# Optimization experiments

Measured on AMD Instinct MI355X. Metric: run time of the kernel, lower is better.

Reference implementation:

```python
import jax, jax.numpy as jnp
import numpy as np

B, H, W, C = 16, 56, 56, 384
NH, WS = 12, 7
N = WS * WS
NW = (H // WS) * (W // WS)
SHIFTS = (0, WS // 2)
HD = C // NH
SCALE = HD ** -0.5


def _rel_idx():
    ch, cw = np.meshgrid(np.arange(WS), np.arange(WS), indexing='ij')
    cf = np.stack([ch.ravel(), cw.ravel()])            # (2, N)
    rc = cf[:, :, None] - cf[:, None, :]               # (2, N, N)
    rc = rc.transpose(1, 2, 0).copy()
    rc[:, :, 0] += WS - 1
    rc[:, :, 1] += WS - 1
    rc[:, :, 0] *= 2 * WS - 1
    return rc.sum(-1).astype(np.int32)                 # (N, N)


def _attn_mask(shift):
    img = np.zeros((H, W))
    sl = (slice(0, -WS), slice(-WS, -shift), slice(-shift, None))
    cnt = 0
    for hs in sl:
        for ws_ in sl:
            img[hs, ws_] = cnt
            cnt += 1
    mw = img.reshape(H // WS, WS, W // WS, WS).transpose(0, 2, 1, 3).reshape(-1, N)
    d = mw[:, None, :] - mw[:, :, None]
    return np.where(d != 0, -100.0, 0.0).astype(np.float32)  # (NW, N, N)


def setup_inputs() -> dict:
    key = jax.random.key(0)
    ks = jax.random.split(key, 8)
    p = lambda k, shape: (jax.random.normal(k, shape, jnp.float32) * 0.02)
    return dict(
        x=jax.random.normal(ks[0], (B, H, W, C), jnp.float32),
        attn_mask=jnp.asarray(_attn_mask(SHIFTS[1])),
        rel_idx=jnp.asarray(_rel_idx()),
        norm1_g=jnp.ones((2, C), jnp.float32),
        norm1_b=jnp.zeros((2, C), jnp.float32),
        qkv_w=p(ks[1], (2, 3 * C, C)),
        qkv_b=jnp.zeros((2, 3 * C), jnp.float32),
        rpb=p(ks[2], (2, (2 * WS - 1) ** 2, NH)),
        proj_w=p(ks[3], (2, C, C)),
        proj_b=jnp.zeros((2, C), jnp.float32),
        norm2_g=jnp.ones((2, C), jnp.float32),
        norm2_b=jnp.zeros((2, C), jnp.float32),
        fc1_w=p(ks[4], (2, 4 * C, C)),
        fc1_b=jnp.zeros((2, 4 * C), jnp.float32),
        fc2_w=p(ks[5], (2, C, 4 * C)),
        fc2_b=jnp.zeros((2, C), jnp.float32),
    )


def _ln(x, g, b):
    m = x.mean(-1, keepdims=True)
    v = x.var(-1, keepdims=True)
    return (x - m) * jax.lax.rsqrt(v + 1e-5) * g + b


def _partition(x):
    # (B,H,W,C) -> (B*nW, N, C)
    x = x.reshape(B, H // WS, WS, W // WS, WS, C)
    return x.transpose(0, 1, 3, 2, 4, 5).reshape(-1, N, C)


def _reverse(w):
    # (B*nW, N, C) -> (B,H,W,C)
    w = w.reshape(B, H // WS, W // WS, WS, WS, C)
    return w.transpose(0, 1, 3, 2, 4, 5).reshape(B, H, W, C)


def reference(x, attn_mask, rel_idx, norm1_g, norm1_b, qkv_w, qkv_b, rpb,
              proj_w, proj_b, norm2_g, norm2_b, fc1_w, fc1_b, fc2_w, fc2_b):
    for i, shift in enumerate(SHIFTS):
        shortcut = x.reshape(B, H * W, C)
        xn = _ln(shortcut, norm1_g[i], norm1_b[i]).reshape(B, H, W, C)
        if shift > 0:
            xn = jnp.roll(xn, (-shift, -shift), (1, 2))
        xw = _partition(xn)                               # (B_, N, C)
        qkv = xw @ qkv_w[i].T + qkv_b[i]                  # (B_, N, 3C)
        qkv = qkv.reshape(-1, N, 3, NH, HD).transpose(2, 0, 3, 1, 4)
        q, k, v = qkv[0], qkv[1], qkv[2]                  # (B_, NH, N, HD)
        attn = jnp.einsum('bhnd,bhmd->bhnm', q * SCALE, k)
        bias = rpb[i][rel_idx.reshape(-1)].reshape(N, N, NH).transpose(2, 0, 1)
        attn = attn + bias[None]
        if shift > 0:
            attn = attn.reshape(B, NW, NH, N, N) + attn_mask[None, :, None]
            attn = attn.reshape(-1, NH, N, N)
        attn = jax.nn.softmax(attn, axis=-1)
        out = jnp.einsum('bhnm,bhmd->bhnd', attn, v)
        out = out.transpose(0, 2, 1, 3).reshape(-1, N, C)
        out = out @ proj_w[i].T + proj_b[i]
        sx = _reverse(out)
        if shift > 0:
            sx = jnp.roll(sx, (shift, shift), (1, 2))
        x = shortcut + sx.reshape(B, H * W, C)
        h = jax.nn.gelu(_ln(x, norm2_g[i], norm2_b[i]) @ fc1_w[i].T + fc1_b[i],
                        approximate=False)
        x = x + (h @ fc2_w[i].T + fc2_b[i])
        x = x.reshape(B, H, W, C)
    return x
```

## Files before the change

### kernel.cpp

```cpp
#include <hip/hip_runtime.h>
#include <hip/hip_fp8.h>
#include <math.h>

typedef unsigned char  u8;
typedef unsigned short u16;
typedef unsigned int   u32;
typedef long long      i64;
typedef __attribute__((ext_vector_type(4))) float f32x4;
typedef __attribute__((ext_vector_type(8))) short bf16x8;

#define M_TOK 50176
#define CDIM  384

__device__ __forceinline__ u16 f2b(float f){
  union { float f; u32 u; } v; v.f = f;
  u32 r = v.u + 0x7fffu + ((v.u >> 16) & 1u);
  return (u16)(r >> 16);
}
__device__ __forceinline__ u32 pack2(float a, float b){
  return (u32)f2b(a) | ((u32)f2b(b) << 16);
}
__device__ __forceinline__ u8 f2q(float v){
  __hip_fp8_e4m3 t(v);
  return *reinterpret_cast<u8*>(&t);
}

__device__ __forceinline__ void gload_lds16(const void* g, void* l){
  __builtin_amdgcn_global_load_lds((const __attribute__((address_space(1))) u32*)g,
                                   (__attribute__((address_space(3))) u32*)l, 16, 0, 0);
}

__global__ void cvtw(const float* __restrict__ in, u16* __restrict__ out, int n4){
  int i = blockIdx.x * 256 + threadIdx.x;
  if (i < n4){
    float4 v = ((const float4*)in)[i];
    uint2 o; o.x = pack2(v.x, v.y); o.y = pack2(v.z, v.w);
    ((uint2*)out)[i] = o;
  }
}
__global__ void cvtw8(const float* __restrict__ in, u8* __restrict__ out, int n4){
  int i = blockIdx.x * 256 + threadIdx.x;
  if (i < n4){
    float4 v = ((const float4*)in)[i];
    u32 o = (u32)f2q(v.x) | ((u32)f2q(v.y) << 8) |
            ((u32)f2q(v.z) << 16) | ((u32)f2q(v.w) << 24);
    ((u32*)out)[i] = o;
  }
}

template<int F8>
__global__ __launch_bounds__(256) void ln_kernel(
    const float* __restrict__ x, const float* __restrict__ g,
    const float* __restrict__ b, void* __restrict__ out, int ntok)
{
  int wave = threadIdx.x >> 6, lane = threadIdx.x & 63;
  for (long t = blockIdx.x * 4 + wave; t < ntok; t += (long)gridDim.x * 4){
    const float* xr = x + t * CDIM;
    float v[6]; float s = 0.f, ss = 0.f;
    #pragma unroll
    for (int j = 0; j < 6; ++j){ v[j] = xr[j*64 + lane]; s += v[j]; ss += v[j]*v[j]; }
    #pragma unroll
    for (int o = 32; o >= 1; o >>= 1){ s += __shfl_xor(s, o); ss += __shfl_xor(ss, o); }
    float mean = s * (1.f/384.f);
    float var  = ss * (1.f/384.f) - mean*mean;
    float rs   = rsqrtf(var + 1e-5f);
    #pragma unroll
    for (int j = 0; j < 6; ++j){
      int c = j*64 + lane;
      float val = (v[j] - mean) * rs * g[c] + b[c];
      if (F8) ((u8*)out)[t*CDIM + c] = f2q(val);
      else    ((u16*)out)[t*CDIM + c] = f2b(val);
    }
  }
}

template<int EPI>
__global__ __launch_bounds__(256, 4) void gemm_bt(
    const u16* __restrict__ A, const u16* __restrict__ Wt,
    const float* __restrict__ bias, const float* __restrict__ resid,
    void* __restrict__ outp, int M, int N, int K)
{
  __shared__ __align__(16) u16 smem[16384];
  const int tid  = threadIdx.x;
  const int wave = tid >> 6, lane = tid & 63;
  const int nbn  = N >> 7;
  const int nwg = gridDim.x;
  const int q8 = nwg >> 3, r8 = nwg & 7, xcd = blockIdx.x & 7, o8 = blockIdx.x >> 3;
  const int sid = (xcd < r8 ? xcd*(q8+1) : r8*(q8+1) + (xcd-r8)*q8) + o8;
  const int bm = sid / nbn, bn = sid % nbn;
  const int wr = wave >> 1, wc = wave & 1;
  const int l15 = lane & 15, l4 = lane >> 4;
  const int srow = tid >> 2, sch = tid & 3;

  f32x4 acc[4][4] = {};

  auto STAGE = [&](int buf, int kt){
    u16* lAp = smem + buf*4096;
    u16* lBp = smem + 8192 + buf*4096;
    #pragma unroll
    for (int it = 0; it < 2; ++it){
      int row = it*64 + srow;
      int chs = sch ^ ((srow >> 1) & 3);
      const u16* ga = A  + (size_t)(bm*128 + row) * K + kt + chs*8;
      const u16* gb = Wt + (size_t)(bn*128 + row) * K + kt + chs*8;
      gload_lds16(ga, &lAp[(it*256 + wave*64) * 8]);
      gload_lds16(gb, &lBp[(it*256 + wave*64) * 8]);
    }
  };

  const int NK = K >> 5;
  STAGE(0, 0);

  int cur = 0;
  for (int ki = 0; ki < NK; ++ki){
    if (ki + 1 < NK){
      STAGE(cur ^ 1, (ki + 1) * 32);
      asm volatile("s_waitcnt vmcnt(4)" ::: "memory");
    } else {
      asm volatile("s_waitcnt vmcnt(0)" ::: "memory");
    }
    __builtin_amdgcn_s_barrier();
    const u16* lAp = smem + cur*4096;
    const u16* lBp = smem + 8192 + cur*4096;
    bf16x8 af[4], bfr[4];
    const int rc = (l4 ^ ((l15 >> 1) & 3)) * 8;
    #pragma unroll
    for (int mi = 0; mi < 4; ++mi)
      af[mi] = *(const bf16x8*)&lAp[(wr*64 + mi*16 + l15)*32 + rc];
    #pragma unroll
    for (int ni = 0; ni < 4; ++ni)
      bfr[ni] = *(const bf16x8*)&lBp[(wc*64 + ni*16 + l15)*32 + rc];
    #pragma unroll
    for (int mi = 0; mi < 4; ++mi)
      #pragma unroll
      for (int ni = 0; ni < 4; ++ni)
        acc[mi][ni] = __builtin_amdgcn_mfma_f32_16x16x32_bf16(af[mi], bfr[ni], acc[mi][ni], 0, 0, 0);
    __builtin_amdgcn_s_barrier();
    cur ^= 1;
  }

  if (EPI == 2){
    #pragma unroll
    for (int ni = 0; ni < 4; ++ni){
      int col = bn*128 + wc*64 + ni*16 + l15;
      float bb = bias[col];
      #pragma unroll
      for (int mi = 0; mi < 4; ++mi){
        int row0 = bm*128 + wr*64 + mi*16 + l4*4;
        #pragma unroll
        for (int r = 0; r < 4; ++r){
          long off = (long)(row0 + r) * N + col;
          ((float*)outp)[off] = resid[off] + acc[mi][ni][r] + bb;
        }
      }
    }
  } else {
    #pragma unroll
    for (int ni = 0; ni < 4; ++ni){
      int colL = wc*64 + ni*16 + l15;
      float bb = bias[bn*128 + colL];
      int colS = colL ^ (l4*16);
      #pragma unroll
      for (int mi = 0; mi < 4; ++mi){
        int rowL = wr*64 + mi*16 + l4*4;
        #pragma unroll
        for (int r = 0; r < 4; ++r){
          float v = acc[mi][ni][r] + bb;
          smem[(rowL + r)*128 + colS] = f2b(v);
        }
      }
    }
    __syncthreads();
    const u32* eb = (const u32*)smem;
    u32* og = (u32*)outp;
    const int nW = N >> 1;
    #pragma unroll
    for (int it = 0; it < 32; ++it){
      int row = wave*32 + it;
      u32 w = eb[row*64 + (lane ^ (((row >> 2) & 3) * 8))];
      __builtin_nontemporal_store(w, &og[(size_t)(bm*128 + row) * nW + bn*64 + lane]);
    }
  }
}

template<int EPI>
__global__ __launch_bounds__(256, 4) void gemm_f8(
    const u8* __restrict__ A, const u8* __restrict__ Wt,
    const float* __restrict__ bias, const float* __restrict__ resid,
    void* __restrict__ outp, int M, int N, int K)
{
  __shared__ __align__(16) u8 smem[17408];
  const int tid  = threadIdx.x;
  const int wave = tid >> 6, lane = tid & 63;
  const int nbn  = N >> 7;
  const int nwg = gridDim.x;
  const int q8 = nwg >> 3, r8 = nwg & 7, xcd = blockIdx.x & 7, o8 = blockIdx.x >> 3;
  const int sid = (xcd < r8 ? xcd*(q8+1) : r8*(q8+1) + (xcd-r8)*q8) + o8;
  const int bm = sid / nbn, bn = sid % nbn;
  const int wr = wave >> 1, wc = wave & 1;
  const int l15 = lane & 15, l4 = lane >> 4;

  f32x4 acc[4][4] = {};

  const int gsl = tid ^ ((tid >> 3) & 7);
  const int grow = gsl >> 1, gc16 = gsl & 1;

  auto STAGE = [&](int buf, int kt){
    const u8* ga = A  + (size_t)(bm*128 + grow) * K + kt + gc16*16;
    const u8* gb = Wt + (size_t)(bn*128 + grow) * K + kt + gc16*16;
    gload_lds16(ga, &smem[buf*8192 + tid*16]);
    gload_lds16(gb, &smem[buf*8192 + 4096 + tid*16]);
  };

  const int NK = K >> 5;
  STAGE(0, 0);

  const int c16 = l4 >> 1, half8 = (l4 & 1) * 8;
  int spA[4], spB[4];
  #pragma unroll
  for (int mi = 0; mi < 4; ++mi){
    int s = (wr*64 + mi*16 + l15)*2 + c16;
    spA[mi] = (s ^ ((s >> 3) & 7)) * 16 + half8;
  }
  #pragma unroll
  for (int ni = 0; ni < 4; ++ni){
    int s = (wc*64 + ni*16 + l15)*2 + c16;
    spB[ni] = (s ^ ((s >> 3) & 7)) * 16 + half8;
  }

  int cur = 0;
  for (int ki = 0; ki < NK; ++ki){
    if (ki + 1 < NK){
      STAGE(cur ^ 1, (ki + 1) * 32);
      asm volatile("s_waitcnt vmcnt(2)" ::: "memory");
    } else {
      asm volatile("s_waitcnt vmcnt(0)" ::: "memory");
    }
    __builtin_amdgcn_s_barrier();
    const u8* lAp = smem + cur*8192;
    const u8* lBp = smem + cur*8192 + 4096;
    i64 af[4], bf[4];
    #pragma unroll
    for (int mi = 0; mi < 4; ++mi)
      af[mi] = *(const i64*)&lAp[spA[mi]];
    #pragma unroll
    for (int ni = 0; ni < 4; ++ni)
      bf[ni] = *(const i64*)&lBp[spB[ni]];
    #pragma unroll
    for (int mi = 0; mi < 4; ++mi)
      #pragma unroll
      for (int ni = 0; ni < 4; ++ni)
        acc[mi][ni] = __builtin_amdgcn_mfma_f32_16x16x32_fp8_fp8(af[mi], bf[ni], acc[mi][ni], 0, 0, 0);
    __builtin_amdgcn_s_barrier();
    cur ^= 1;
  }

  if (EPI == 2){
    #pragma unroll
    for (int ni = 0; ni < 4; ++ni){
      int col = bn*128 + wc*64 + ni*16 + l15;
      float bb = bias[col];
      #pragma unroll
      for (int mi = 0; mi < 4; ++mi){
        int row0 = bm*128 + wr*64 + mi*16 + l4*4;
        #pragma unroll
        for (int r = 0; r < 4; ++r){
          long off = (long)(row0 + r) * N + col;
          ((float*)outp)[off] = resid[off] + acc[mi][ni][r] + bb;
        }
      }
    }
  } else {
    #pragma unroll
    for (int ni = 0; ni < 4; ++ni){
      int col = wc*64 + ni*16 + l15;
      float bb = bias[bn*128 + col];
      #pragma unroll
      for (int mi = 0; mi < 4; ++mi){
        int row0 = wr*64 + mi*16 + l4*4;
        #pragma unroll
        for (int r = 0; r < 4; ++r){
          float v = acc[mi][ni][r] + bb;
          v = 0.5f * v * (1.f + erff(v * 0.70710678118654752f));
          smem[(row0 + r)*132 + col] = f2q(v);
        }
      }
    }
    __syncthreads();
    u32* og = (u32*)outp;
    const int nW = N >> 2;
    const int colu = tid & 31, rw = tid >> 5;
    #pragma unroll
    for (int it = 0; it < 16; ++it){
      int row = it*8 + rw;
      u32 w = *(const u32*)&smem[row*132 + colu*4];
      __builtin_nontemporal_store(w, &og[(size_t)(bm*128 + row) * nW + bn*32 + colu]);
    }
  }
}

__global__ void build_btbl(const float* __restrict__ rpb, const int* __restrict__ ridx,
                           float* __restrict__ btbl){
  int q = blockIdx.x & 63, h = blockIdx.x >> 6;
  int l = threadIdx.x;
  float v = -1e9f;
  if (q < 49){
    int key = (l & 3) * 16 + (l >> 2);
    if (key < 49) v = rpb[ridx[q*49 + key] * 12 + h];
  }
  btbl[(h*64 + q)*64 + l] = v;
}

template<int SHIFT>
__global__ __launch_bounds__(64) void attn_mfma(
    const u16* __restrict__ qkv, const float* __restrict__ btbl,
    u16* __restrict__ attn_out)
{
  __shared__ __align__(16) u16 p_lds[64*72];
  __shared__ __align__(16) u16 vt_lds[32*72];
  __shared__ int tok_lds[64];
  __shared__ int rid_lds[64];

  const int bid = blockIdx.x;
  const int h   = bid % 12;
  const int win = bid / 12;
  const int b   = win >> 6, wl = win & 63;
  const int wy  = wl >> 3,  wx = wl & 7;
  const int lane = threadIdx.x;
  const int l15 = lane & 15, l4 = lane >> 4;

  auto tokof = [&](int n)->int{
    int r = (n * 9363) >> 16;
    int c = n - r * 7;
    int hh = wy*7 + r + SHIFT; if (hh >= 56) hh -= 56;
    int ww = wx*7 + c + SHIFT; if (ww >= 56) ww -= 56;
    return b*3136 + hh*56 + ww;
  };

  {
    const int n  = lane;
    const int nc = n < 49 ? n : 48;
    const int t  = tokof(nc);
    tok_lds[n] = t;
    if (SHIFT){
      int r = (nc * 9363) >> 16, c = nc - r*7;
      int gh = wy*7 + r, gw = wx*7 + c;
      int rh = gh <= 48 ? 0 : (gh <= 52 ? 1 : 2);
      int rw = gw <= 48 ? 0 : (gw <= 52 ? 1 : 2);
      rid_lds[n] = rh*3 + rw;
    }
    const uint4* vp = (const uint4*)(qkv + (size_t)t*1152 + 768 + h*32);
    u32 w[16];
    #pragma unroll
    for (int j4 = 0; j4 < 4; ++j4){
      uint4 u = vp[j4];
      w[j4*4+0]=u.x; w[j4*4+1]=u.y; w[j4*4+2]=u.z; w[j4*4+3]=u.w;
    }
    if (n >= 49){
      #pragma unroll
      for (int j = 0; j < 16; ++j) w[j] = 0;
    }
    #pragma unroll
    for (int j = 0; j < 16; ++j){
      vt_lds[(2*j  )*72 + n] = (u16)(w[j] & 0xffffu);
      vt_lds[(2*j+1)*72 + n] = (u16)(w[j] >> 16);
    }
  }

  bf16x8 qa[4], kb[4];
  #pragma unroll
  for (int mi = 0; mi < 4; ++mi){
    int row = mi*16 + l15; int t = tokof(row < 49 ? row : 48);
    qa[mi] = *(const bf16x8*)(qkv + (size_t)t*1152 + h*32 + l4*8);
  }
  #pragma unroll
  for (int ni = 0; ni < 4; ++ni){
    int row = ni*16 + l15; int t = tokof(row < 49 ? row : 48);
    kb[ni] = *(const bf16x8*)(qkv + (size_t)t*1152 + 384 + h*32 + l4*8);
  }
  f32x4 s[4][4] = {};
  #pragma unroll
  for (int mi = 0; mi < 4; ++mi)
    #pragma unroll
    for (int ni = 0; ni < 4; ++ni)
      s[mi][ni] = __builtin_amdgcn_mfma_f32_16x16x32_bf16(qa[mi], kb[ni], s[mi][ni], 0, 0, 0);

  __syncthreads();

  int rid_k[4];
  if (SHIFT){
    #pragma unroll
    for (int ni = 0; ni < 4; ++ni) rid_k[ni] = rid_lds[ni*16 + l15];
  }

  const float* bt = btbl + h*4096;
  float den[4][4];
  #pragma unroll
  for (int mi = 0; mi < 4; ++mi){
    #pragma unroll
    for (int r = 0; r < 4; ++r){
      int q = mi*16 + l4*4 + r;
      f32x4 bq = *(const f32x4*)(bt + q*64 + l15*4);
      int ridq = 0;
      if (SHIFT) ridq = rid_lds[q];
      #pragma unroll
      for (int ni = 0; ni < 4; ++ni){
        float v = s[mi][ni][r] * 0.17677669529663687f + bq[ni];
        if (SHIFT) v += (ridq == rid_k[ni]) ? 0.f : -100.f;
        s[mi][ni][r] = v;
      }
      float m0 = fmaxf(fmaxf(s[mi][0][r], s[mi][1][r]), fmaxf(s[mi][2][r], s[mi][3][r]));
      #pragma unroll
      for (int o = 1; o <= 8; o <<= 1) m0 = fmaxf(m0, __shfl_xor(m0, o));
      float d0 = 0.f;
      #pragma unroll
      for (int ni = 0; ni < 4; ++ni){
        float e = __expf(s[mi][ni][r] - m0);
        s[mi][ni][r] = e; d0 += e;
      }
      #pragma unroll
      for (int o = 1; o <= 8; o <<= 1) d0 += __shfl_xor(d0, o);
      den[mi][r] = d0;
    }
  }

  #pragma unroll
  for (int mi = 0; mi < 4; ++mi)
    #pragma unroll
    for (int r = 0; r < 4; ++r){
      int q = mi*16 + l4*4 + r;
      #pragma unroll
      for (int ni = 0; ni < 4; ++ni)
        p_lds[q*72 + ni*16 + l15] = f2b(s[mi][ni][r]);
    }

  __syncthreads();

  f32x4 o2[4][2] = {};
  #pragma unroll
  for (int ks = 0; ks < 2; ++ks){
    bf16x8 vb[2];
    #pragma unroll
    for (int ni = 0; ni < 2; ++ni)
      vb[ni] = *(const bf16x8*)&vt_lds[(ni*16 + l15)*72 + ks*32 + l4*8];
    #pragma unroll
    for (int mi = 0; mi < 4; ++mi){
      bf16x8 pa = *(const bf16x8*)&p_lds[(mi*16 + l15)*72 + ks*32 + l4*8];
      #pragma unroll
      for (int ni = 0; ni < 2; ++ni)
        o2[mi][ni] = __builtin_amdgcn_mfma_f32_16x16x32_bf16(pa, vb[ni], o2[mi][ni], 0, 0, 0);
    }
  }

  #pragma unroll
  for (int mi = 0; mi < 4; ++mi){
    #pragma unroll
    for (int r = 0; r < 4; ++r){
      int q = mi*16 + l4*4 + r;
      if (q < 49){
        float inv = 1.f / den[mi][r];
        long t = tok_lds[q];
        #pragma unroll
        for (int ni = 0; ni < 2; ++ni){
          int d = ni*16 + l15;
          attn_out[t*384 + h*32 + d] = f2b(o2[mi][ni][r] * inv);
        }
      }
    }
  }
}

extern "C" void kernel_launch(void* const* d_in, const int* in_sizes, int n_in,
                              void* d_out, int out_size, void* d_ws, size_t ws_size,
                              hipStream_t stream)
{
  const float* x_in   = (const float*)d_in[0];
  const int*   relidx = (const int*)d_in[2];
  const float* n1g    = (const float*)d_in[3];
  const float* n1b    = (const float*)d_in[4];
  const float* qkvw   = (const float*)d_in[5];
  const float* qkvb   = (const float*)d_in[6];
  const float* rpb    = (const float*)d_in[7];
  const float* pw     = (const float*)d_in[8];
  const float* pb     = (const float*)d_in[9];
  const float* n2g    = (const float*)d_in[10];
  const float* n2b    = (const float*)d_in[11];
  const float* f1w    = (const float*)d_in[12];
  const float* f1b    = (const float*)d_in[13];
  const float* f2w    = (const float*)d_in[14];
  const float* f2bb   = (const float*)d_in[15];
  float* xout = (float*)d_out;

  char* ws = (char*)d_ws;
  u16* wqkv   = (u16*)ws; ws += (size_t)2*1152*384*2;
  u16* wproj  = (u16*)ws; ws += (size_t)2*384*384*2;
  u8*  wfc1q  = (u8*)ws;  ws += (size_t)2*1536*384;
  u8*  wfc2q  = (u8*)ws;  ws += (size_t)2*384*1536;
  u16* bufA   = (u16*)ws; ws += (size_t)M_TOK*1536*2;
  u16* bufB   = (u16*)ws; ws += (size_t)M_TOK*384*2;
  u8*  bufD   = (u8*)ws;  ws += (size_t)M_TOK*384;
  float* btbl = (float*)(bufA + (size_t)M_TOK*1152);
  u8* h8 = (u8*)bufA;

  {
    int n;
    n = 2*1152*384;  cvtw <<<dim3((n/4+255)/256), dim3(256), 0, stream>>>(qkvw, wqkv,  n/4);
    n = 2*384*384;   cvtw <<<dim3((n/4+255)/256), dim3(256), 0, stream>>>(pw,   wproj, n/4);
    n = 2*1536*384;  cvtw8<<<dim3((n/4+255)/256), dim3(256), 0, stream>>>(f1w,  wfc1q, n/4);
    n = 2*384*1536;  cvtw8<<<dim3((n/4+255)/256), dim3(256), 0, stream>>>(f2w,  wfc2q, n/4);
  }

  for (int i = 0; i < 2; ++i){
    const float* xi = (i == 0) ? x_in : xout;
    ln_kernel<0><<<dim3(2048), dim3(256), 0, stream>>>(xi, n1g + i*384, n1b + i*384, bufB, M_TOK);
    gemm_bt<0><<<dim3(3528), dim3(256), 0, stream>>>(
        bufB, wqkv + (size_t)i*1152*384, qkvb + i*1152, nullptr, bufA, M_TOK, 1152, 384);
    build_btbl<<<dim3(768), dim3(64), 0, stream>>>(rpb + (size_t)i*169*12, relidx, btbl);
    if (i == 0)
      attn_mfma<0><<<dim3(12288), dim3(64), 0, stream>>>(bufA, btbl, bufB);
    else
      attn_mfma<3><<<dim3(12288), dim3(64), 0, stream>>>(bufA, btbl, bufB);
    gemm_bt<2><<<dim3(1176), dim3(256), 0, stream>>>(
        bufB, wproj + (size_t)i*384*384, pb + i*384, xi, xout, M_TOK, 384, 384);
    ln_kernel<1><<<dim3(2048), dim3(256), 0, stream>>>(xout, n2g + i*384, n2b + i*384, bufD, M_TOK);
    gemm_f8<1><<<dim3(4704), dim3(256), 0, stream>>>(
        bufD, wfc1q + (size_t)i*1536*384, f1b + i*1536, nullptr, h8, M_TOK, 1536, 384);
    gemm_f8<2><<<dim3(1176), dim3(256), 0, stream>>>(
        h8, wfc2q + (size_t)i*384*1536, f2bb + i*384, xout, xout, M_TOK, 384, 1536);
  }
  (void)in_sizes; (void)n_in; (void)out_size; (void)ws_size;
}
```

Measured before the change: 929.1 us.

## Store fc1 GELU output directly with permuted fc2 weight layout, tanh GELU

The fc1 epilogue now packs four fp8 GELU outputs per lane straight into a 32-bit global store instead of staging through shared memory and a barrier. The packed columns are interleaved with stride 16, so the fc2 fp8 weights are re-laid out with a matching permutation along K to keep the contraction correct. The exact erf GELU is replaced by the tanh approximation using a fast exp, which cuts epilogue ALU work but slightly changes numerics. The global stores become 4-byte scattered per lane rather than row-coalesced, which may hurt write efficiency.

```diff
diff --git a/kernel.cpp b/kernel.cpp
--- a/kernel.cpp
+++ b/kernel.cpp
@@ -23,6 +23,12 @@
 __device__ __forceinline__ u8 f2q(float v){
   __hip_fp8_e4m3 t(v);
   return *reinterpret_cast<u8*>(&t);
+}
+__device__ __forceinline__ float gelu(float x){
+  float u = x * (0.7978845608028654f + 0.035677408136300125f * x * x);
+  float e = __expf(2.f * u);
+  float th = 1.f - 2.f / (e + 1.f);
+  return 0.5f * x * (1.f + th);
 }
 
 __device__ __forceinline__ void gload_lds16(const void* g, void* l){
@@ -45,6 +51,19 @@
     u32 o = (u32)f2q(v.x) | ((u32)f2q(v.y) << 8) |
             ((u32)f2q(v.z) << 16) | ((u32)f2q(v.w) << 24);
     ((u32*)out)[i] = o;
+  }
+}
+__global__ void cvtw8p(const float* __restrict__ in, u8* __restrict__ out,
+                       int rows, int cols){
+  int idx = blockIdx.x * 256 + threadIdx.x;
+  if (idx < rows * (cols >> 2)){
+    int byte0 = idx << 2;
+    int row = byte0 / cols, cb = byte0 % cols;
+    int g = cb >> 6, s = (cb & 63) >> 2;
+    const float* rp = in + (size_t)row * cols + g*64;
+    u32 w = (u32)f2q(rp[s]) | ((u32)f2q(rp[16 + s]) << 8) |
+            ((u32)f2q(rp[32 + s]) << 16) | ((u32)f2q(rp[48 + s]) << 24);
+    ((u32*)out)[idx] = w;
   }
 }
 
@@ -189,7 +208,7 @@
     const float* __restrict__ bias, const float* __restrict__ resid,
     void* __restrict__ outp, int M, int N, int K)
 {
-  __shared__ __align__(16) u8 smem[17408];
+  __shared__ __align__(16) u8 smem[16384];
   const int tid  = threadIdx.x;
   const int wave = tid >> 6, lane = tid & 63;
   const int nbn  = N >> 7;
@@ -271,30 +290,25 @@
       }
     }
   } else {
-    #pragma unroll
-    for (int ni = 0; ni < 4; ++ni){
-      int col = wc*64 + ni*16 + l15;
-      float bb = bias[bn*128 + col];
-      #pragma unroll
-      for (int mi = 0; mi < 4; ++mi){
-        int row0 = wr*64 + mi*16 + l4*4;
-        #pragma unroll
-        for (int r = 0; r < 4; ++r){
-          float v = acc[mi][ni][r] + bb;
-          v = 0.5f * v * (1.f + erff(v * 0.70710678118654752f));
-          smem[(row0 + r)*132 + col] = f2q(v);
-        }
-      }
-    }
-    __syncthreads();
     u32* og = (u32*)outp;
     const int nW = N >> 2;
-    const int colu = tid & 31, rw = tid >> 5;
-    #pragma unroll
-    for (int it = 0; it < 16; ++it){
-      int row = it*8 + rw;
-      u32 w = *(const u32*)&smem[row*132 + colu*4];
-      __builtin_nontemporal_store(w, &og[(size_t)(bm*128 + row) * nW + bn*32 + colu]);
+    float bb[4];
+    #pragma unroll
+    for (int ni = 0; ni < 4; ++ni) bb[ni] = bias[bn*128 + wc*64 + ni*16 + l15];
+    const int wordc = (bn*128 + wc*64 + l15*4) >> 2;
+    #pragma unroll
+    for (int mi = 0; mi < 4; ++mi){
+      int row0 = bm*128 + wr*64 + mi*16 + l4*4;
+      #pragma unroll
+      for (int r = 0; r < 4; ++r){
+        u32 w = 0;
+        #pragma unroll
+        for (int ni = 0; ni < 4; ++ni){
+          float v = gelu(acc[mi][ni][r] + bb[ni]);
+          w |= (u32)f2q(v) << (8*ni);
+        }
+        __builtin_nontemporal_store(w, &og[(size_t)(row0 + r) * nW + wordc]);
+      }
     }
   }
 }
@@ -504,10 +518,10 @@
 
   {
     int n;
-    n = 2*1152*384;  cvtw <<<dim3((n/4+255)/256), dim3(256), 0, stream>>>(qkvw, wqkv,  n/4);
-    n = 2*384*384;   cvtw <<<dim3((n/4+255)/256), dim3(256), 0, stream>>>(pw,   wproj, n/4);
-    n = 2*1536*384;  cvtw8<<<dim3((n/4+255)/256), dim3(256), 0, stream>>>(f1w,  wfc1q, n/4);
-    n = 2*384*1536;  cvtw8<<<dim3((n/4+255)/256), dim3(256), 0, stream>>>(f2w,  wfc2q, n/4);
+    n = 2*1152*384;  cvtw  <<<dim3((n/4+255)/256), dim3(256), 0, stream>>>(qkvw, wqkv,  n/4);
+    n = 2*384*384;   cvtw  <<<dim3((n/4+255)/256), dim3(256), 0, stream>>>(pw,   wproj, n/4);
+    n = 2*1536*384;  cvtw8 <<<dim3((n/4+255)/256), dim3(256), 0, stream>>>(f1w,  wfc1q, n/4);
+    n = 2*384*1536;  cvtw8p<<<dim3((n/4+255)/256), dim3(256), 0, stream>>>(f2w,  wfc2q, 2*384, 1536);
   }
 
   for (int i = 0; i < 2; ++i){
```

Result: no change. 939.8 us (+1.1%).
